# Kernel optimization log

Measured on AMD Instinct MI355X. Metric: run time of the kernel, lower is better.

Reference implementation:

```python
import jax, jax.numpy as jnp
import numpy as np

B, S, D, H, HD = 2, 4096, 768, 12, 64
W = 256          # one-sided window (attention_window=512)
G = 128          # number of global tokens (prefix)
NB = S // W      # sequence blocks
EPS = 1e-5


def _heads(x, w, b):
    # [B,S,D] -> [B,H,S,HD]
    return (x @ w + b).reshape(B, S, H, HD).transpose(0, 2, 1, 3)


def _blocks(xp):
    # xp: [B,H,S+2W,HD] (padded by W on both sides) -> [B,H,NB,3W,HD]
    # block n holds keys/values at absolute positions [n*W - W, n*W + 2W)
    return jnp.concatenate(
        [xp[:, :, j * W:j * W + S].reshape(B, H, NB, W, HD) for j in range(3)], axis=3)


def setup_inputs() -> dict:
    key = jax.random.key(0)
    ks = jax.random.split(key, 12)
    p = lambda i, shape: jax.random.normal(ks[i], shape, jnp.float32) * 0.02
    z = lambda n: jnp.zeros((n,), jnp.float32)
    return {
        'hidden_states': jax.random.normal(ks[0], (B, S, D), jnp.float32),
        'attention_mask': jnp.zeros((B, S), jnp.float32),  # 0 = local attention, no padding
        'is_index_global_attn': jnp.broadcast_to(jnp.arange(S) < G, (B, S)),
        'Wq': p(1, (D, D)), 'bq': z(D),
        'Wk': p(2, (D, D)), 'bk': z(D),
        'Wv': p(3, (D, D)), 'bv': z(D),
        'Wqg': p(4, (D, D)), 'bqg': z(D),
        'Wkg': p(5, (D, D)), 'bkg': z(D),
        'Wvg': p(6, (D, D)), 'bvg': z(D),
        'Wo': p(7, (D, D)), 'bo': z(D),
        'ln_gamma': jnp.ones((D,), jnp.float32),
        'ln_beta': jnp.zeros((D,), jnp.float32),
    }


def reference(hidden_states, attention_mask, is_index_global_attn,
              Wq, bq, Wk, bk, Wv, bv, Wqg, bqg, Wkg, bkg, Wvg, bvg,
              Wo, bo, ln_gamma, ln_beta):
    scale = 1.0 / np.sqrt(HD)
    q = _heads(hidden_states, Wq, bq) * scale   # [B,H,S,HD]
    k = _heads(hidden_states, Wk, bk)
    v = _heads(hidden_states, Wv, bv)

    pad = ((0, 0), (0, 0), (W, W), (0, 0))
    kb = _blocks(jnp.pad(k, pad))                # [B,H,NB,3W,HD]
    vb = _blocks(jnp.pad(v, pad))
    qb = q.reshape(B, H, NB, W, HD)
    s_band = jnp.einsum('bhnqd,bhnkd->bhnqk', qb, kb)   # [B,H,NB,W,3W]

    # band + boundary mask; global keys are removed from windowed attention
    # (they appear as dedicated prepended columns instead, as in HF Longformer)
    qi = jnp.arange(W)[:, None]                  # query offset in block
    kk = jnp.arange(3 * W)[None, :]              # key offset in 3W window
    rel = kk - W - qi                            # [W,3W] relative position
    kpos = jnp.arange(NB)[:, None, None] * W + (kk - W)[None]  # [NB,W(1),3W] absolute key pos
    valid = (jnp.abs(rel) <= W)[None] & (kpos >= G) & (kpos < S)  # [NB,W,3W]
    s_band = jnp.where(valid[None, None], s_band, -1e9)

    # global key columns (regular k/v projections, per HF Longformer)
    kg, vg = k[:, :, :G], v[:, :, :G]
    s_glob = jnp.einsum('bhsd,bhgd->bhsg', q, kg)        # [B,H,S,G]
    scores = jnp.concatenate([s_glob, s_band.reshape(B, H, S, 3 * W)], axis=-1)
    probs = jax.nn.softmax(scores, axis=-1)
    p_glob = probs[..., :G]
    p_band = probs[..., G:].reshape(B, H, NB, W, 3 * W)
    out = (jnp.einsum('bhnqk,bhnkd->bhnqd', p_band, vb).reshape(B, H, S, HD)
           + jnp.einsum('bhsg,bhgd->bhsd', p_glob, vg))

    # global query tokens attend to everything via the *_global projections;
    # their outputs overwrite the windowed outputs (HF behavior)
    qg = _heads(hidden_states, Wqg, bqg)[:, :, :G] * scale
    kgf = _heads(hidden_states, Wkg, bkg)
    vgf = _heads(hidden_states, Wvg, bvg)
    pg = jax.nn.softmax(jnp.einsum('bhgd,bhsd->bhgs', qg, kgf), axis=-1)
    og = jnp.einsum('bhgs,bhsd->bhgd', pg, vgf)
    out = out.at[:, :, :G].set(og)

    # TFLongformerSelfOutput: dense + residual + LayerNorm
    ctx = out.transpose(0, 2, 1, 3).reshape(B, S, D)
    y = ctx @ Wo + bo + hidden_states
    mu = y.mean(-1, keepdims=True)
    var = ((y - mu) ** 2).mean(-1, keepdims=True)
    return (y - mu) / jnp.sqrt(var + EPS) * ln_gamma + ln_beta
```

## Files before the change

kernel.cpp:

```cpp
#include <hip/hip_runtime.h>
#include <stdint.h>

#define BB 2
#define SS 4096
#define DD 768
#define HH 12
#define HDD 64
#define WW 256
#define GG 128
#define NBB 16
#define NSPLIT 16

typedef __attribute__((ext_vector_type(4))) float f32x4;
typedef __attribute__((ext_vector_type(8))) short bf16x8;
typedef __attribute__((ext_vector_type(4))) short s16x4;
typedef __attribute__((ext_vector_type(4))) unsigned short u16x4;

__device__ __forceinline__ unsigned short f2bf(float x) {
  union { float f; unsigned int u; } v; v.f = x;
  return (unsigned short)((v.u + 0x7fffu + ((v.u >> 16) & 1u)) >> 16);
}

__device__ __forceinline__ void async16(void* lds, const void* g) {
  __builtin_amdgcn_global_load_lds(
      (const __attribute__((address_space(1))) unsigned int*)g,
      (__attribute__((address_space(3))) unsigned int*)lds, 16, 0, 0);
}

__device__ __forceinline__ uint32_t lds_b(const void* p) {
  return (uint32_t)(uintptr_t)(__attribute__((address_space(3))) const void*)p;
}

__device__ __forceinline__ s16x4 tr_read(uint32_t addr) {
  s16x4 d;
  asm volatile("ds_read_b64_tr_b16 %0, %1" : "=v"(d) : "v"(addr) : "memory");
  return d;
}

__global__ __launch_bounds__(256) void k_cvt(const float* __restrict__ x,
                                             unsigned short* __restrict__ o, int n4) {
  int i = blockIdx.x * 256 + threadIdx.x;
  if (i >= n4) return;
  f32x4 v = ((const f32x4*)x)[i];
  u16x4 r;
  r[0] = f2bf(v[0]); r[1] = f2bf(v[1]); r[2] = f2bf(v[2]); r[3] = f2bf(v[3]);
  ((u16x4*)o)[i] = r;
}

struct WArgs {
  const float* s[7];
  unsigned short* d[7];
};
__global__ __launch_bounds__(256) void k_tw(WArgs a) {
  __shared__ float t[64][65];
  const float* src = a.s[blockIdx.z];
  unsigned short* dst = a.d[blockIdx.z];
  int n0 = blockIdx.x * 64, k0 = blockIdx.y * 64;
#pragma unroll
  for (int it = 0; it < 16; ++it) {
    int idx = it * 256 + threadIdx.x;
    int r = idx >> 6, c = idx & 63;
    t[r][c] = src[(size_t)(k0 + r) * DD + n0 + c];
  }
  __syncthreads();
#pragma unroll
  for (int it = 0; it < 16; ++it) {
    int idx = it * 256 + threadIdx.x;
    int r = idx >> 6, c = idx & 63;
    dst[(size_t)(n0 + r) * DD + k0 + c] = f2bf(t[c][r]);
  }
}

template <int OMODE>
__global__ __launch_bounds__(256) void k_gemm(
    const unsigned short* __restrict__ A, const unsigned short* __restrict__ Wt,
    const float* __restrict__ b0, const float* __restrict__ b1,
    const float* __restrict__ b2, const float* __restrict__ b3,
    const float* __restrict__ b4, unsigned short* __restrict__ outH,
    float* __restrict__ outY, const float* __restrict__ resid) {
  const int bm = blockIdx.x;
  int bn, p;
  if (OMODE == 0) { p = blockIdx.y / 6; bn = blockIdx.y % 6; }
  else { p = 0; bn = blockIdx.y; }
  const float* bias = b0;
  if (OMODE == 0) bias = (p == 0) ? b0 : (p == 1) ? b1 : (p == 2) ? b2 : (p == 3) ? b3 : b4;
  const float scale = (OMODE == 1 || (OMODE == 0 && p == 0)) ? 0.125f : 1.0f;

  __shared__ unsigned short Asm_[128 * 64];
  __shared__ unsigned short Bsm_[128 * 64];
  const int tid = threadIdx.x;
  const int l = tid & 63, w = tid >> 6;
  const int wr = w >> 1, wc = w & 1;
  const int g = l >> 4, ln = l & 15;
  const int l3 = l >> 3, l7 = l & 7;
  const int slotsrc = l7 ^ l3;

  f32x4 zf = {0.f, 0.f, 0.f, 0.f};
  f32x4 acc[4][4];
#pragma unroll
  for (int i = 0; i < 4; ++i)
#pragma unroll
    for (int j = 0; j < 4; ++j) acc[i][j] = zf;

  const int wtrow0 = (OMODE == 0 ? p * DD : 0) + bn * 128;

  for (int kt = 0; kt < 12; ++kt) {
#pragma unroll
    for (int i = 0; i < 4; ++i) {
      int u = i * 4 + w;
      int row = u * 8 + l3;
      int ar = bm * 128 + row;
      if (OMODE == 1) ar = ((ar >> 7) << 12) + (ar & 127);
      async16(&Asm_[u * 512], A + (size_t)ar * DD + kt * 64 + slotsrc * 8);
      async16(&Bsm_[u * 512], Wt + (size_t)(wtrow0 + row) * DD + kt * 64 + slotsrc * 8);
    }
    __syncthreads();
#pragma unroll
    for (int kc = 0; kc < 2; ++kc) {
      bf16x8 af[4], bfr[4];
#pragma unroll
      for (int t = 0; t < 4; ++t) {
        int arow = wr * 64 + t * 16 + ln;
        af[t] = *(const bf16x8*)&Asm_[arow * 64 + (((kc * 4 + g) ^ (arow & 7)) << 3)];
        int brow = wc * 64 + t * 16 + ln;
        bfr[t] = *(const bf16x8*)&Bsm_[brow * 64 + (((kc * 4 + g) ^ (brow & 7)) << 3)];
      }
#pragma unroll
      for (int ti = 0; ti < 4; ++ti)
#pragma unroll
        for (int tj = 0; tj < 4; ++tj)
          acc[ti][tj] = __builtin_amdgcn_mfma_f32_16x16x32_bf16(af[ti], bfr[tj], acc[ti][tj], 0, 0, 0);
    }
    __syncthreads();
  }

#pragma unroll
  for (int tj = 0; tj < 4; ++tj) {
    int nl = bn * 128 + wc * 64 + tj * 16 + ln;
    float bv = bias[nl];
#pragma unroll
    for (int ti = 0; ti < 4; ++ti) {
#pragma unroll
      for (int r = 0; r < 4; ++r) {
        int m = bm * 128 + wr * 64 + ti * 16 + g * 4 + r;
        float val = acc[ti][tj][r] + bv;
        if (OMODE == 2) {
          outY[(size_t)m * DD + nl] = val + resid[(size_t)m * DD + nl];
        } else if (OMODE == 0) {
          val *= scale;
          int b = m >> 12, s = m & 4095, h = nl >> 6, d = nl & 63;
          outH[(size_t)p * (BB * HH * SS * HDD) +
               (((size_t)(b * HH + h) * SS + s) * HDD) + d] = f2bf(val);
        } else {
          val *= scale;
          int b = m >> 7, gi = m & 127, h = nl >> 6, d = nl & 63;
          outH[(((size_t)(b * HH + h) * GG + gi) * HDD) + d] = f2bf(val);
        }
      }
    }
  }
}

template <int MODE>
__global__ __launch_bounds__(512) void k_attn(
    const unsigned short* __restrict__ qbuf, const unsigned short* __restrict__ kbuf,
    const unsigned short* __restrict__ vbuf, unsigned short* __restrict__ ctx,
    float* __restrict__ Opart, float* __restrict__ mlp) {
  constexpr int TQ = (MODE == 0) ? 2 : 1;
  constexpr int MAXCH = (MODE == 0) ? 14 : 4;

  __shared__ unsigned short Ksm[2][64 * 64];
  __shared__ unsigned short Vsm[2][64 * 64];
  __shared__ unsigned short Psm[8][16 * 64];

  const int tid = threadIdx.x;
  const int l = tid & 63, w = tid >> 6;
  const int g = l >> 4, ln = l & 15;
  const int l3 = l >> 3, l7 = l & 7;

  int b, h, n, split;
  if (MODE == 0) {
    n = blockIdx.x & 15; h = (blockIdx.x >> 4) % 12; b = blockIdx.x / (16 * 12); split = 0;
  } else {
    split = blockIdx.x & 15; int bhid = blockIdx.x >> 4; h = bhid % 12; b = bhid / 12; n = 0;
  }

  const size_t bh = (size_t)(b * HH + h);
  const unsigned short* qp = qbuf + bh * (size_t)((MODE == 0) ? SS * HDD : GG * HDD);
  const unsigned short* kp = kbuf + bh * (size_t)(SS * HDD);
  const unsigned short* vp = vbuf + bh * (size_t)(SS * HDD);

  int kbs[MAXCH]; int nch = 0;
  if (MODE == 0) {
    kbs[nch++] = 0; kbs[nch++] = 64;
#pragma unroll
    for (int j = 0; j < 12; ++j) {
      int kb = n * 256 - 256 + j * 64;
      if (kb >= GG && kb < SS) kbs[nch++] = kb;
    }
  } else {
#pragma unroll
    for (int i = 0; i < 4; ++i) kbs[nch++] = (split * 4 + i) * 64;
  }

  const int qrow0 = (MODE == 0) ? (n * 256 + w * 32) : (w * 16);

  bf16x8 qf[TQ][2];
#pragma unroll
  for (int t = 0; t < TQ; ++t)
#pragma unroll
    for (int kc = 0; kc < 2; ++kc)
      qf[t][kc] = *(const bf16x8*)&qp[(size_t)(qrow0 + t * 16 + ln) * HDD + kc * 32 + g * 8];

  f32x4 zf = {0.f, 0.f, 0.f, 0.f};
  f32x4 o[TQ][4];
  float mrun[TQ][4], lrun[TQ][4];
#pragma unroll
  for (int t = 0; t < TQ; ++t) {
#pragma unroll
    for (int dj = 0; dj < 4; ++dj) o[t][dj] = zf;
#pragma unroll
    for (int r = 0; r < 4; ++r) { mrun[t][r] = -1e30f; lrun[t][r] = 0.f; }
  }

  const uint32_t vbase = lds_b(Vsm);
  const int vwoff = (((tid >> 3) >> 2) << 8) | (((tid & 7) >> 1) << 6) |
                    (((tid >> 3) & 3) << 4) | ((tid & 1) << 3);

  bf16x8 vv;
  {
    int kb = kbs[0];
    async16(&Ksm[0][w * 512], kp + (size_t)(kb + w * 8 + l3) * HDD + (size_t)((l7 ^ l3) << 3));
    vv = *(const bf16x8*)&vp[(size_t)(kb + (tid >> 3)) * HDD + (size_t)((tid & 7) << 3)];
  }
  int buf = 0;

  for (int ci = 0; ci < nch; ++ci) {
    const int kbase = kbs[ci];
    asm volatile("s_waitcnt vmcnt(0)" ::: "memory");
    *(bf16x8*)&Vsm[buf][vwoff] = vv;
    __syncthreads();

    bf16x8 vnext;
    if (ci + 1 < nch) {
      int kb = kbs[ci + 1];
      async16(&Ksm[buf ^ 1][w * 512],
              kp + (size_t)(kb + w * 8 + l3) * HDD + (size_t)((l7 ^ l3) << 3));
      vnext = *(const bf16x8*)&vp[(size_t)(kb + (tid >> 3)) * HDD + (size_t)((tid & 7) << 3)];
    }

    f32x4 sc[TQ][4];
#pragma unroll
    for (int t = 0; t < TQ; ++t)
#pragma unroll
      for (int cj = 0; cj < 4; ++cj) sc[t][cj] = zf;
#pragma unroll
    for (int kc = 0; kc < 2; ++kc) {
      bf16x8 kf[4];
#pragma unroll
      for (int cj = 0; cj < 4; ++cj) {
        int key = cj * 16 + ln;
        kf[cj] = *(const bf16x8*)&Ksm[buf][key * 64 + (((kc * 4 + g) ^ (key & 7)) << 3)];
      }
#pragma unroll
      for (int t = 0; t < TQ; ++t)
#pragma unroll
        for (int cj = 0; cj < 4; ++cj)
          sc[t][cj] = __builtin_amdgcn_mfma_f32_16x16x32_bf16(qf[t][kc], kf[cj], sc[t][cj], 0, 0, 0);
    }

    if (MODE == 0 && kbase >= GG) {
      const int koff = kbase - (n * 256 - 256);
#pragma unroll
      for (int t = 0; t < TQ; ++t)
#pragma unroll
        for (int cj = 0; cj < 4; ++cj) {
          int kk = koff + cj * 16 + ln;
#pragma unroll
          for (int r = 0; r < 4; ++r) {
            int qi = w * 32 + t * 16 + g * 4 + r;
            if (!(kk >= qi && kk <= qi + 2 * WW)) sc[t][cj][r] = -1e9f;
          }
        }
    }

    float alpha[TQ][4];
#pragma unroll
    for (int t = 0; t < TQ; ++t)
#pragma unroll
      for (int r = 0; r < 4; ++r) {
        float m4 = fmaxf(fmaxf(sc[t][0][r], sc[t][1][r]), fmaxf(sc[t][2][r], sc[t][3][r]));
#pragma unroll
        for (int d = 1; d < 16; d <<= 1) m4 = fmaxf(m4, __shfl_xor(m4, d, 64));
        float mnew = fmaxf(mrun[t][r], m4);
        float al = __expf(mrun[t][r] - mnew);
        mrun[t][r] = mnew;
        float rs = 0.f;
#pragma unroll
        for (int cj = 0; cj < 4; ++cj) {
          float pv = __expf(sc[t][cj][r] - mnew);
          sc[t][cj][r] = pv;
          rs += pv;
        }
#pragma unroll
        for (int d = 1; d < 16; d <<= 1) rs += __shfl_xor(rs, d, 64);
        lrun[t][r] = lrun[t][r] * al + rs;
        alpha[t][r] = al;
      }

#pragma unroll
    for (int t = 0; t < TQ; ++t)
#pragma unroll
      for (int dj = 0; dj < 4; ++dj)
#pragma unroll
        for (int r = 0; r < 4; ++r) o[t][dj][r] *= alpha[t][r];

    const uint32_t vb = vbase + (uint32_t)(buf << 13);
#pragma unroll
    for (int t = 0; t < TQ; ++t) {
#pragma unroll
      for (int cj = 0; cj < 4; ++cj) {
        int pcol = cj * 16 + ln;
#pragma unroll
        for (int r = 0; r < 4; ++r) {
          int prow = g * 4 + r;
          Psm[w][prow * 64 + (((pcol >> 3) ^ (prow & 7)) << 3) + (pcol & 7)] =
              f2bf(sc[t][cj][r]);
        }
      }
#pragma unroll
      for (int kc = 0; kc < 2; ++kc) {
        s16x4 vlo[4], vhi[4];
#pragma unroll
        for (int dj = 0; dj < 4; ++dj) {
          uint32_t a = vb + (uint32_t)((((kc * 8 + g * 2) * 256) + dj * 64 + ln) * 2);
          vlo[dj] = tr_read(a);
          vhi[dj] = tr_read(a + 512);
        }
        bf16x8 pa = *(const bf16x8*)&Psm[w][ln * 64 + (((kc * 4 + g) ^ (ln & 7)) << 3)];
        asm volatile("s_waitcnt lgkmcnt(0)" ::: "memory");
        __builtin_amdgcn_sched_barrier(0);
#pragma unroll
        for (int dj = 0; dj < 4; ++dj) {
          bf16x8 vf = __builtin_shufflevector(vlo[dj], vhi[dj], 0, 1, 2, 3, 4, 5, 6, 7);
          o[t][dj] = __builtin_amdgcn_mfma_f32_16x16x32_bf16(pa, vf, o[t][dj], 0, 0, 0);
        }
      }
    }

    vv = vnext;
    buf ^= 1;
  }

  if (MODE == 0) {
#pragma unroll
    for (int t = 0; t < TQ; ++t)
#pragma unroll
      for (int r = 0; r < 4; ++r) {
        float inv = 1.f / lrun[t][r];
        int spos = qrow0 + t * 16 + g * 4 + r;
#pragma unroll
        for (int dj = 0; dj < 4; ++dj) {
          int dcol = dj * 16 + ln;
          ctx[((size_t)b * SS + spos) * DD + h * HDD + dcol] = f2bf(o[t][dj][r] * inv);
        }
      }
  } else {
#pragma unroll
    for (int r = 0; r < 4; ++r) {
      int q = w * 16 + g * 4 + r;
      size_t base = (((bh * NSPLIT + split) * GG) + q) * (size_t)HDD;
#pragma unroll
      for (int dj = 0; dj < 4; ++dj) Opart[base + dj * 16 + ln] = o[0][dj][r];
      if (ln == 0) {
        size_t mb = (((bh * NSPLIT + split) * GG) + q) * 2;
        mlp[mb] = mrun[0][r];
        mlp[mb + 1] = lrun[0][r];
      }
    }
  }
}

__global__ __launch_bounds__(256) void k_red(const float* __restrict__ Opart,
                                             const float* __restrict__ mlp,
                                             unsigned short* __restrict__ ctx) {
  int wid = blockIdx.x * 4 + (threadIdx.x >> 6);
  int d = threadIdx.x & 63;
  int bh = wid >> 7, q = wid & 127;
  int b = bh / HH, h = bh % HH;

  float mmax = -1e30f;
#pragma unroll
  for (int s = 0; s < NSPLIT; ++s)
    mmax = fmaxf(mmax, mlp[(((size_t)bh * NSPLIT + s) * GG + q) * 2]);
  float acc = 0.f, denom = 0.f;
#pragma unroll
  for (int s = 0; s < NSPLIT; ++s) {
    size_t mb = (((size_t)bh * NSPLIT + s) * GG + q) * 2;
    float wgt = __expf(mlp[mb] - mmax);
    denom += wgt * mlp[mb + 1];
    acc += wgt * Opart[(((size_t)bh * NSPLIT + s) * GG + q) * HDD + d];
  }
  ctx[((size_t)b * SS + q) * DD + h * HDD + d] = f2bf(acc / denom);
}

__global__ __launch_bounds__(256) void k_ln(const float* __restrict__ Y,
                                            const float* __restrict__ gam,
                                            const float* __restrict__ bet,
                                            float* __restrict__ outp) {
  const int row = blockIdx.x;
  const float* y = Y + (size_t)row * DD;
  float v0 = y[threadIdx.x], v1 = y[threadIdx.x + 256], v2 = y[threadIdx.x + 512];
  float s = v0 + v1 + v2, s2 = v0 * v0 + v1 * v1 + v2 * v2;
#pragma unroll
  for (int d = 1; d < 64; d <<= 1) { s += __shfl_xor(s, d, 64); s2 += __shfl_xor(s2, d, 64); }
  __shared__ float r1[4], r2[4];
  int w = threadIdx.x >> 6, l = threadIdx.x & 63;
  if (l == 0) { r1[w] = s; r2[w] = s2; }
  __syncthreads();
  s = r1[0] + r1[1] + r1[2] + r1[3];
  s2 = r2[0] + r2[1] + r2[2] + r2[3];
  float mu = s * (1.f / 768.f);
  float var = s2 * (1.f / 768.f) - mu * mu;
  float rstd = rsqrtf(var + 1e-5f);
  float* op = outp + (size_t)row * DD;
  op[threadIdx.x] = (v0 - mu) * rstd * gam[threadIdx.x] + bet[threadIdx.x];
  op[threadIdx.x + 256] = (v1 - mu) * rstd * gam[threadIdx.x + 256] + bet[threadIdx.x + 256];
  op[threadIdx.x + 512] = (v2 - mu) * rstd * gam[threadIdx.x + 512] + bet[threadIdx.x + 512];
}

extern "C" void kernel_launch(void* const* d_in, const int* in_sizes, int n_in,
                              void* d_out, int out_size, void* d_ws, size_t ws_size,
                              hipStream_t stream) {
  const float* hidden = (const float*)d_in[0];
  const float* Wq = (const float*)d_in[3];  const float* bq = (const float*)d_in[4];
  const float* Wk = (const float*)d_in[5];  const float* bk = (const float*)d_in[6];
  const float* Wv = (const float*)d_in[7];  const float* bv = (const float*)d_in[8];
  const float* Wqg = (const float*)d_in[9]; const float* bqg = (const float*)d_in[10];
  const float* Wkg = (const float*)d_in[11]; const float* bkg = (const float*)d_in[12];
  const float* Wvg = (const float*)d_in[13]; const float* bvg = (const float*)d_in[14];
  const float* Wo = (const float*)d_in[15]; const float* bo = (const float*)d_in[16];
  const float* gam = (const float*)d_in[17]; const float* bet = (const float*)d_in[18];

  char* ws = (char*)d_ws;
  const size_t SZH = (size_t)BB * HH * SS * HDD;
  unsigned short* xb = (unsigned short*)(ws);
  unsigned short* Wt5 = (unsigned short*)(ws + 12582912);
  unsigned short* Wtqg = (unsigned short*)(ws + 12582912 + 5898240);
  unsigned short* Wto = (unsigned short*)(ws + 12582912 + 5898240 + 1179648);
  unsigned short* qkv = (unsigned short*)(ws + 20840448);
  unsigned short* qg = (unsigned short*)(ws + 20840448 + 62914560);
  float* Opart = (float*)(ws + 84148224);
  float* mlp = (float*)(ws + 84148224 + 12582912);
  unsigned short* ctx = xb;
  float* Y = (float*)qkv;

  k_cvt<<<dim3((BB * SS * DD / 4 + 255) / 256), dim3(256), 0, stream>>>(hidden, xb, BB * SS * DD / 4);

  WArgs wa;
  wa.s[0] = Wq; wa.s[1] = Wk; wa.s[2] = Wv; wa.s[3] = Wkg; wa.s[4] = Wvg; wa.s[5] = Wqg; wa.s[6] = Wo;
  wa.d[0] = Wt5; wa.d[1] = Wt5 + 589824; wa.d[2] = Wt5 + 2 * 589824;
  wa.d[3] = Wt5 + 3 * 589824; wa.d[4] = Wt5 + 4 * 589824;
  wa.d[5] = Wtqg; wa.d[6] = Wto;
  k_tw<<<dim3(12, 12, 7), dim3(256), 0, stream>>>(wa);

  k_gemm<0><<<dim3(64, 30), dim3(256), 0, stream>>>(xb, Wt5, bq, bk, bv, bkg, bvg, qkv, nullptr, nullptr);
  k_gemm<1><<<dim3(2, 6), dim3(256), 0, stream>>>(xb, Wtqg, bqg, nullptr, nullptr, nullptr, nullptr, qg, nullptr, nullptr);

  k_attn<1><<<dim3(BB * HH * NSPLIT), dim3(512), 0, stream>>>(qg, qkv + 3 * SZH, qkv + 4 * SZH,
                                                              nullptr, Opart, mlp);
  k_attn<0><<<dim3(BB * HH * NBB), dim3(512), 0, stream>>>(qkv, qkv + SZH, qkv + 2 * SZH,
                                                           ctx, nullptr, nullptr);
  k_red<<<dim3(BB * HH * GG / 4), dim3(256), 0, stream>>>(Opart, mlp, ctx);

  k_gemm<2><<<dim3(64, 6), dim3(256), 0, stream>>>(ctx, Wto, bo, nullptr, nullptr, nullptr, nullptr, nullptr, Y, hidden);

  k_ln<<<dim3(BB * SS), dim3(256), 0, stream>>>(Y, gam, bet, (float*)d_out);
}
```

Before: 372.5 us.

## Rewrite attention kernel with 32x32 MFMA and register-resident P via permlane swaps

Switches the attention kernel from 16x16x32 MFMA tiles to 32x32x16 bf16 MFMA, computing S^T so the probabilities can be packed into A operands in registers with v_cvt_pk_bf16 and permlane32_swap, removing the P round-trip through LDS. Softmax moves to the exp2 domain with a folded log2e scale, the per-row rescale factors are shared through a small LDS table, and the global-query variant runs with 4 waves at 32 rows each, staging two rows of K/V per thread. It also adds s_setprio around the MFMA blocks and simplifies the chunk list into an arithmetic formula. The larger accumulator tiles raise register pressure, and the lane-layout remapping is easy to get wrong.

Result: faster. 322.8 us (-13.4%).

```diff
diff --git a/kernel.cpp b/kernel.cpp
--- a/kernel.cpp
+++ b/kernel.cpp
@@ -12,6 +12,7 @@
 #define NSPLIT 16
 
 typedef __attribute__((ext_vector_type(4))) float f32x4;
+typedef __attribute__((ext_vector_type(16))) float f32x16;
 typedef __attribute__((ext_vector_type(8))) short bf16x8;
 typedef __attribute__((ext_vector_type(4))) short s16x4;
 typedef __attribute__((ext_vector_type(4))) unsigned short u16x4;
@@ -35,6 +36,23 @@
   s16x4 d;
   asm volatile("ds_read_b64_tr_b16 %0, %1" : "=v"(d) : "v"(addr) : "memory");
   return d;
+}
+
+__device__ __forceinline__ unsigned int cvtpk(float lo, float hi) {
+  unsigned int d;
+  asm("v_cvt_pk_bf16_f32 %0, %1, %2" : "=v"(d) : "v"(lo), "v"(hi));
+  return d;
+}
+
+__device__ __forceinline__ void plswap(int& a, int& b) {
+  auto r = __builtin_amdgcn_permlane32_swap(a, b, false, false);
+  a = r[0]; b = r[1];
+}
+
+__device__ __forceinline__ float xhalf(float x, int hi) {
+  int a = __float_as_int(x), b = a;
+  auto r = __builtin_amdgcn_permlane32_swap(a, b, false, false);
+  return __int_as_float(hi ? r[0] : r[1]);
 }
 
 __global__ __launch_bounds__(256) void k_cvt(const float* __restrict__ x,
@@ -162,20 +180,21 @@
 }
 
 template <int MODE>
-__global__ __launch_bounds__(512) void k_attn(
+__global__ __launch_bounds__((MODE == 0) ? 512 : 256, 4) void k_attn(
     const unsigned short* __restrict__ qbuf, const unsigned short* __restrict__ kbuf,
     const unsigned short* __restrict__ vbuf, unsigned short* __restrict__ ctx,
     float* __restrict__ Opart, float* __restrict__ mlp) {
-  constexpr int TQ = (MODE == 0) ? 2 : 1;
-  constexpr int MAXCH = (MODE == 0) ? 14 : 4;
+  constexpr int NW = (MODE == 0) ? 8 : 4;
+  constexpr int NSTG = (MODE == 0) ? 1 : 2;
+  constexpr float L2E = 1.4426950408889634f;
 
   __shared__ unsigned short Ksm[2][64 * 64];
   __shared__ unsigned short Vsm[2][64 * 64];
-  __shared__ unsigned short Psm[8][16 * 64];
+  __shared__ __align__(16) float Alds[NW][32];
 
   const int tid = threadIdx.x;
   const int l = tid & 63, w = tid >> 6;
-  const int g = l >> 4, ln = l & 15;
+  const int l31 = l & 31, hi = l >> 5;
   const int l3 = l >> 3, l7 = l & 7;
 
   int b, h, n, split;
@@ -190,195 +209,199 @@
   const unsigned short* kp = kbuf + bh * (size_t)(SS * HDD);
   const unsigned short* vp = vbuf + bh * (size_t)(SS * HDD);
 
-  int kbs[MAXCH]; int nch = 0;
+  int bstart = 0, nch;
   if (MODE == 0) {
-    kbs[nch++] = 0; kbs[nch++] = 64;
-#pragma unroll
-    for (int j = 0; j < 12; ++j) {
-      int kb = n * 256 - 256 + j * 64;
-      if (kb >= GG && kb < SS) kbs[nch++] = kb;
-    }
+    bstart = n * 256 - 256;
+    int s0 = bstart < GG ? GG : bstart;
+    int e0 = bstart + 768; if (e0 > SS) e0 = SS;
+    nch = 2 + ((e0 - s0) >> 6);
+    bstart = s0;
   } else {
-#pragma unroll
-    for (int i = 0; i < 4; ++i) kbs[nch++] = (split * 4 + i) * 64;
-  }
-
-  const int qrow0 = (MODE == 0) ? (n * 256 + w * 32) : (w * 16);
-
-  bf16x8 qf[TQ][2];
-#pragma unroll
-  for (int t = 0; t < TQ; ++t)
-#pragma unroll
-    for (int kc = 0; kc < 2; ++kc)
-      qf[t][kc] = *(const bf16x8*)&qp[(size_t)(qrow0 + t * 16 + ln) * HDD + kc * 32 + g * 8];
-
-  f32x4 zf = {0.f, 0.f, 0.f, 0.f};
-  f32x4 o[TQ][4];
-  float mrun[TQ][4], lrun[TQ][4];
-#pragma unroll
-  for (int t = 0; t < TQ; ++t) {
-#pragma unroll
-    for (int dj = 0; dj < 4; ++dj) o[t][dj] = zf;
-#pragma unroll
-    for (int r = 0; r < 4; ++r) { mrun[t][r] = -1e30f; lrun[t][r] = 0.f; }
-  }
+    nch = 4;
+  }
+  const int qrow0 = (MODE == 0) ? (n * 256 + w * 32) : (w * 32);
+
+  bf16x8 qf[4];
+#pragma unroll
+  for (int kd = 0; kd < 4; ++kd)
+    qf[kd] = *(const bf16x8*)&qp[(size_t)(qrow0 + l31) * HDD + kd * 16 + hi * 8];
+
+  f32x16 O[2];
+#pragma unroll
+  for (int dt = 0; dt < 2; ++dt)
+#pragma unroll
+    for (int r = 0; r < 16; ++r) O[dt][r] = 0.f;
+  float m2 = -1e30f, lsum = 0.f;
 
   const uint32_t vbase = lds_b(Vsm);
-  const int vwoff = (((tid >> 3) >> 2) << 8) | (((tid & 7) >> 1) << 6) |
-                    (((tid >> 3) & 3) << 4) | ((tid & 1) << 3);
-
-  bf16x8 vv;
+  int vwoff[NSTG];
   {
-    int kb = kbs[0];
-    async16(&Ksm[0][w * 512], kp + (size_t)(kb + w * 8 + l3) * HDD + (size_t)((l7 ^ l3) << 3));
-    vv = *(const bf16x8*)&vp[(size_t)(kb + (tid >> 3)) * HDD + (size_t)((tid & 7) << 3)];
+    int key0 = tid >> 3, dc = tid & 7;
+#pragma unroll
+    for (int u = 0; u < NSTG; ++u) {
+      int key = u * 32 + key0;
+      vwoff[u] = (((key >> 2) << 8) | ((dc >> 1) << 6) | ((key & 3) << 4) | ((dc & 1) << 3));
+    }
+  }
+
+#define KB_OF(ci) ((ci) < 2 && MODE == 0 ? (ci) * 64 : (MODE == 0 ? bstart + ((ci) - 2) * 64 : ((split * 4 + (ci)) * 64)))
+
+  bf16x8 vv[NSTG];
+  {
+    int kb = KB_OF(0);
+#pragma unroll
+    for (int u = 0; u < NSTG; ++u) {
+      async16(&Ksm[0][(u * NW + w) * 512],
+              kp + (size_t)(kb + (u * NW + w) * 8 + l3) * HDD + ((l7 ^ l3) << 3));
+      vv[u] = *(const bf16x8*)&vp[(size_t)(kb + u * 32 + (tid >> 3)) * HDD + ((tid & 7) << 3)];
+    }
   }
   int buf = 0;
 
   for (int ci = 0; ci < nch; ++ci) {
-    const int kbase = kbs[ci];
+    const int kbase = KB_OF(ci);
     asm volatile("s_waitcnt vmcnt(0)" ::: "memory");
-    *(bf16x8*)&Vsm[buf][vwoff] = vv;
+#pragma unroll
+    for (int u = 0; u < NSTG; ++u) *(bf16x8*)&Vsm[buf][vwoff[u]] = vv[u];
     __syncthreads();
 
-    bf16x8 vnext;
     if (ci + 1 < nch) {
-      int kb = kbs[ci + 1];
-      async16(&Ksm[buf ^ 1][w * 512],
-              kp + (size_t)(kb + w * 8 + l3) * HDD + (size_t)((l7 ^ l3) << 3));
-      vnext = *(const bf16x8*)&vp[(size_t)(kb + (tid >> 3)) * HDD + (size_t)((tid & 7) << 3)];
-    }
-
-    f32x4 sc[TQ][4];
-#pragma unroll
-    for (int t = 0; t < TQ; ++t)
-#pragma unroll
-      for (int cj = 0; cj < 4; ++cj) sc[t][cj] = zf;
-#pragma unroll
-    for (int kc = 0; kc < 2; ++kc) {
-      bf16x8 kf[4];
-#pragma unroll
-      for (int cj = 0; cj < 4; ++cj) {
-        int key = cj * 16 + ln;
-        kf[cj] = *(const bf16x8*)&Ksm[buf][key * 64 + (((kc * 4 + g) ^ (key & 7)) << 3)];
-      }
-#pragma unroll
-      for (int t = 0; t < TQ; ++t)
-#pragma unroll
-        for (int cj = 0; cj < 4; ++cj)
-          sc[t][cj] = __builtin_amdgcn_mfma_f32_16x16x32_bf16(qf[t][kc], kf[cj], sc[t][cj], 0, 0, 0);
-    }
+      int kb = KB_OF(ci + 1);
+#pragma unroll
+      for (int u = 0; u < NSTG; ++u) {
+        async16(&Ksm[buf ^ 1][(u * NW + w) * 512],
+                kp + (size_t)(kb + (u * NW + w) * 8 + l3) * HDD + ((l7 ^ l3) << 3));
+        vv[u] = *(const bf16x8*)&vp[(size_t)(kb + u * 32 + (tid >> 3)) * HDD + ((tid & 7) << 3)];
+      }
+    }
+
+    f32x16 sc[2];
+#pragma unroll
+    for (int s = 0; s < 2; ++s)
+#pragma unroll
+      for (int r = 0; r < 16; ++r) sc[s][r] = 0.f;
+    __builtin_amdgcn_s_setprio(1);
+#pragma unroll
+    for (int kd = 0; kd < 4; ++kd) {
+#pragma unroll
+      for (int s = 0; s < 2; ++s) {
+        int row = s * 32 + l31;
+        bf16x8 kf = *(const bf16x8*)&Ksm[buf][row * 64 + ((((kd << 1) + hi) ^ (row & 7)) << 3)];
+        sc[s] = __builtin_amdgcn_mfma_f32_32x32x16_bf16(kf, qf[kd], sc[s], 0, 0, 0);
+      }
+    }
+    __builtin_amdgcn_s_setprio(0);
 
     if (MODE == 0 && kbase >= GG) {
-      const int koff = kbase - (n * 256 - 256);
-#pragma unroll
-      for (int t = 0; t < TQ; ++t)
-#pragma unroll
-        for (int cj = 0; cj < 4; ++cj) {
-          int kk = koff + cj * 16 + ln;
-#pragma unroll
-          for (int r = 0; r < 4; ++r) {
-            int qi = w * 32 + t * 16 + g * 4 + r;
-            if (!(kk >= qi && kk <= qi + 2 * WW)) sc[t][cj][r] = -1e9f;
-          }
+      const int base0 = (kbase - (n * 256 - 256)) - (w * 32 + l31);
+#pragma unroll
+      for (int s = 0; s < 2; ++s)
+#pragma unroll
+        for (int r = 0; r < 16; ++r) {
+          int t = base0 + s * 32 + (r & 3) + 8 * (r >> 2) + 4 * hi;
+          if ((unsigned)t > 512u) sc[s][r] = -1e9f;
         }
     }
 
-    float alpha[TQ][4];
-#pragma unroll
-    for (int t = 0; t < TQ; ++t)
-#pragma unroll
-      for (int r = 0; r < 4; ++r) {
-        float m4 = fmaxf(fmaxf(sc[t][0][r], sc[t][1][r]), fmaxf(sc[t][2][r], sc[t][3][r]));
-#pragma unroll
-        for (int d = 1; d < 16; d <<= 1) m4 = fmaxf(m4, __shfl_xor(m4, d, 64));
-        float mnew = fmaxf(mrun[t][r], m4);
-        float al = __expf(mrun[t][r] - mnew);
-        mrun[t][r] = mnew;
-        float rs = 0.f;
-#pragma unroll
-        for (int cj = 0; cj < 4; ++cj) {
-          float pv = __expf(sc[t][cj][r] - mnew);
-          sc[t][cj][r] = pv;
-          rs += pv;
-        }
-#pragma unroll
-        for (int d = 1; d < 16; d <<= 1) rs += __shfl_xor(rs, d, 64);
-        lrun[t][r] = lrun[t][r] * al + rs;
-        alpha[t][r] = al;
-      }
-
-#pragma unroll
-    for (int t = 0; t < TQ; ++t)
-#pragma unroll
-      for (int dj = 0; dj < 4; ++dj)
-#pragma unroll
-        for (int r = 0; r < 4; ++r) o[t][dj][r] *= alpha[t][r];
+    float mh = sc[0][0];
+#pragma unroll
+    for (int s = 0; s < 2; ++s)
+#pragma unroll
+      for (int r = 0; r < 16; ++r) if (s || r) mh = fmaxf(mh, sc[s][r]);
+    mh = fmaxf(mh, xhalf(mh, hi));
+    float mnew = fmaxf(m2, mh * L2E);
+    float alpha = exp2f(m2 - mnew);
+    m2 = mnew;
+    float sh = 0.f;
+#pragma unroll
+    for (int s = 0; s < 2; ++s)
+#pragma unroll
+      for (int r = 0; r < 16; ++r) {
+        float pv = exp2f(__builtin_fmaf(sc[s][r], L2E, -mnew));
+        sc[s][r] = pv;
+        sh += pv;
+      }
+    sh += xhalf(sh, hi);
+    lsum = lsum * alpha + sh;
+
+    if (l < 32) Alds[w][l] = alpha;
+    f32x4 aT[4];
+#pragma unroll
+    for (int g2 = 0; g2 < 4; ++g2) aT[g2] = *(const f32x4*)&Alds[w][g2 * 8 + hi * 4];
+#pragma unroll
+    for (int dt = 0; dt < 2; ++dt)
+#pragma unroll
+      for (int r = 0; r < 16; ++r) O[dt][r] *= aT[r >> 2][r & 3];
+
+    bf16x8 pa[4];
+#pragma unroll
+    for (int kk = 0; kk < 4; ++kk) {
+      const int s = kk >> 1, h8 = (kk & 1) * 8;
+      int x0 = (int)cvtpk(sc[s][h8 + 0], sc[s][h8 + 1]);
+      int x1 = (int)cvtpk(sc[s][h8 + 2], sc[s][h8 + 3]);
+      int y0 = (int)cvtpk(sc[s][h8 + 4], sc[s][h8 + 5]);
+      int y1 = (int)cvtpk(sc[s][h8 + 6], sc[s][h8 + 7]);
+      plswap(x0, y0); plswap(x1, y1);
+      union { int u[4]; bf16x8 v; } pk;
+      pk.u[0] = x0; pk.u[1] = x1; pk.u[2] = y0; pk.u[3] = y1;
+      pa[kk] = pk.v;
+    }
 
     const uint32_t vb = vbase + (uint32_t)(buf << 13);
 #pragma unroll
-    for (int t = 0; t < TQ; ++t) {
-#pragma unroll
-      for (int cj = 0; cj < 4; ++cj) {
-        int pcol = cj * 16 + ln;
-#pragma unroll
-        for (int r = 0; r < 4; ++r) {
-          int prow = g * 4 + r;
-          Psm[w][prow * 64 + (((pcol >> 3) ^ (prow & 7)) << 3) + (pcol & 7)] =
-              f2bf(sc[t][cj][r]);
-        }
-      }
-#pragma unroll
-      for (int kc = 0; kc < 2; ++kc) {
-        s16x4 vlo[4], vhi[4];
-#pragma unroll
-        for (int dj = 0; dj < 4; ++dj) {
-          uint32_t a = vb + (uint32_t)((((kc * 8 + g * 2) * 256) + dj * 64 + ln) * 2);
-          vlo[dj] = tr_read(a);
-          vhi[dj] = tr_read(a + 512);
-        }
-        bf16x8 pa = *(const bf16x8*)&Psm[w][ln * 64 + (((kc * 4 + g) ^ (ln & 7)) << 3)];
-        asm volatile("s_waitcnt lgkmcnt(0)" ::: "memory");
-        __builtin_amdgcn_sched_barrier(0);
-#pragma unroll
-        for (int dj = 0; dj < 4; ++dj) {
-          bf16x8 vf = __builtin_shufflevector(vlo[dj], vhi[dj], 0, 1, 2, 3, 4, 5, 6, 7);
-          o[t][dj] = __builtin_amdgcn_mfma_f32_16x16x32_bf16(pa, vf, o[t][dj], 0, 0, 0);
-        }
-      }
-    }
-
-    vv = vnext;
+    for (int dt = 0; dt < 2; ++dt) {
+      s16x4 t0[4], t1[4];
+#pragma unroll
+      for (int kk = 0; kk < 4; ++kk) {
+        int kg = kk * 4 + hi * 2;
+        int dgrp = dt * 2 + (l31 >> 4);
+        uint32_t a = vb + (uint32_t)((kg * 256 + dgrp * 64 + (l31 & 15)) << 1);
+        t0[kk] = tr_read(a);
+        t1[kk] = tr_read(a + 512);
+      }
+      asm volatile("s_waitcnt lgkmcnt(0)" ::: "memory");
+      __builtin_amdgcn_sched_barrier(0);
+      __builtin_amdgcn_s_setprio(1);
+#pragma unroll
+      for (int kk = 0; kk < 4; ++kk) {
+        bf16x8 vf = __builtin_shufflevector(t0[kk], t1[kk], 0, 1, 2, 3, 4, 5, 6, 7);
+        O[dt] = __builtin_amdgcn_mfma_f32_32x32x16_bf16(pa[kk], vf, O[dt], 0, 0, 0);
+      }
+      __builtin_amdgcn_s_setprio(0);
+    }
+
     buf ^= 1;
   }
 
   if (MODE == 0) {
-#pragma unroll
-    for (int t = 0; t < TQ; ++t)
-#pragma unroll
-      for (int r = 0; r < 4; ++r) {
-        float inv = 1.f / lrun[t][r];
-        int spos = qrow0 + t * 16 + g * 4 + r;
-#pragma unroll
-        for (int dj = 0; dj < 4; ++dj) {
-          int dcol = dj * 16 + ln;
-          ctx[((size_t)b * SS + spos) * DD + h * HDD + dcol] = f2bf(o[t][dj][r] * inv);
-        }
+    if (l < 32) Alds[w][l] = 1.f / lsum;
+    f32x4 iT[4];
+#pragma unroll
+    for (int g2 = 0; g2 < 4; ++g2) iT[g2] = *(const f32x4*)&Alds[w][g2 * 8 + hi * 4];
+#pragma unroll
+    for (int dt = 0; dt < 2; ++dt)
+#pragma unroll
+      for (int r = 0; r < 16; ++r) {
+        int q = qrow0 + (r & 3) + 8 * (r >> 2) + 4 * hi;
+        int d = dt * 32 + l31;
+        ctx[((size_t)b * SS + q) * DD + h * HDD + d] = f2bf(O[dt][r] * iT[r >> 2][r & 3]);
       }
   } else {
-#pragma unroll
-    for (int r = 0; r < 4; ++r) {
-      int q = w * 16 + g * 4 + r;
-      size_t base = (((bh * NSPLIT + split) * GG) + q) * (size_t)HDD;
-#pragma unroll
-      for (int dj = 0; dj < 4; ++dj) Opart[base + dj * 16 + ln] = o[0][dj][r];
-      if (ln == 0) {
-        size_t mb = (((bh * NSPLIT + split) * GG) + q) * 2;
-        mlp[mb] = mrun[0][r];
-        mlp[mb + 1] = lrun[0][r];
-      }
-    }
-  }
+    size_t pb = (bh * NSPLIT + split) * (size_t)GG;
+#pragma unroll
+    for (int dt = 0; dt < 2; ++dt)
+#pragma unroll
+      for (int r = 0; r < 16; ++r) {
+        int q = w * 32 + (r & 3) + 8 * (r >> 2) + 4 * hi;
+        Opart[(pb + q) * HDD + dt * 32 + l31] = O[dt][r];
+      }
+    if (l < 32) {
+      size_t mb = (pb + w * 32 + l) * 2;
+      mlp[mb] = m2;
+      mlp[mb + 1] = lsum;
+    }
+  }
+#undef KB_OF
 }
 
 __global__ __launch_bounds__(256) void k_red(const float* __restrict__ Opart,
@@ -397,7 +420,7 @@
 #pragma unroll
   for (int s = 0; s < NSPLIT; ++s) {
     size_t mb = (((size_t)bh * NSPLIT + s) * GG + q) * 2;
-    float wgt = __expf(mlp[mb] - mmax);
+    float wgt = exp2f(mlp[mb] - mmax);
     denom += wgt * mlp[mb + 1];
     acc += wgt * Opart[(((size_t)bh * NSPLIT + s) * GG + q) * HDD + d];
   }
@@ -467,7 +490,7 @@
   k_gemm<0><<<dim3(64, 30), dim3(256), 0, stream>>>(xb, Wt5, bq, bk, bv, bkg, bvg, qkv, nullptr, nullptr);
   k_gemm<1><<<dim3(2, 6), dim3(256), 0, stream>>>(xb, Wtqg, bqg, nullptr, nullptr, nullptr, nullptr, qg, nullptr, nullptr);
 
-  k_attn<1><<<dim3(BB * HH * NSPLIT), dim3(512), 0, stream>>>(qg, qkv + 3 * SZH, qkv + 4 * SZH,
+  k_attn<1><<<dim3(BB * HH * NSPLIT), dim3(256), 0, stream>>>(qg, qkv + 3 * SZH, qkv + 4 * SZH,
                                                               nullptr, Opart, mlp);
   k_attn<0><<<dim3(BB * HH * NBB), dim3(512), 0, stream>>>(qkv, qkv + SZH, qkv + 2 * SZH,
                                                            ctx, nullptr, nullptr);
```
